# Optimization experiments

Hardware: AMD Instinct MI355X
Metric: run time of the kernel (lower is better)

## Reference

```python
import jax, jax.numpy as jnp
import numpy as np

S, B, E, H = 512, 64, 512, 512  # seq_len, batch, embed_dim, lstm_dim


def setup_inputs() -> dict:
    key = jax.random.key(0)
    ks = jax.random.split(key, 16)
    scale = 0.03

    def W(k):
        return jax.random.normal(k, (E + H, H), jnp.float32) * scale

    return {
        "embedded_tokens": jax.random.normal(ks[0], (S, B, E), jnp.float32),
        "hidden0": jnp.zeros((B, H), jnp.float32),
        "context0": jnp.zeros((B, H), jnp.float32),
        "Wf": W(ks[1]), "bf": jnp.zeros((H,), jnp.float32),
        "Wi": W(ks[2]), "bi": jnp.zeros((H,), jnp.float32),
        "Wo": W(ks[3]), "bo": jnp.zeros((H,), jnp.float32),
        "Wc": W(ks[4]), "bc": jnp.zeros((H,), jnp.float32),
        "Wmf": W(ks[5]), "bmf": jnp.zeros((H,), jnp.float32),
        "Wmi": W(ks[6]), "bmi": jnp.zeros((H,), jnp.float32),
        "seq_lengths": jax.random.randint(ks[7], (B,), 1, S + 1, jnp.int32),
    }


def reference(embedded_tokens, hidden0, context0, Wf, bf, Wi, bi, Wo, bo,
              Wc, bc, Wmf, bmf, Wmi, bmi, seq_lengths):
    # ON-LSTM recurrence, dropout p=0.0 so dropout is identity.
    def step(carry, x_t):
        h, c = carry                                   # [B,H], [B,H]
        z = jnp.concatenate([x_t, h], axis=1)          # [B, E+H]
        ft = jax.nn.sigmoid(z @ Wf + bf)
        it = jax.nn.sigmoid(z @ Wi + bi)
        ot = jax.nn.sigmoid(z @ Wo + bo)
        c_hat = jnp.tanh(z @ Wc + bc)
        mf = jnp.cumsum(jax.nn.softmax(z @ Wmf + bmf, axis=1), axis=1)  # master forget (cumax)
        mi = jnp.cumsum(jax.nn.softmax(z @ Wmi + bmi, axis=1), axis=1)  # master input (cumax)
        wt = mf * mi
        f_hat = ft * wt + (mf - wt)
        i_hat = it * wt + (mi - wt)
        c = f_hat * c + i_hat * c_hat
        h = ot * c
        return (h, c), (h, c)

    (_h, _c), (all_h, all_c) = jax.lax.scan(step, (hidden0, context0), embedded_tokens)
    # gather final valid state per example
    t_idx = seq_lengths - 1                            # [B]
    b_idx = jnp.arange(all_h.shape[1])
    state_hidden = all_h[t_idx, b_idx]                 # [B,H]
    state_context = all_c[t_idx, b_idx]                # [B,H]
    return all_h, state_hidden, state_context
```

## Files before the change

kernel.cpp:

```cpp
#include <hip/hip_runtime.h>

#define S_LEN 512
#define NWG   64
#define COLS  48
#define OUT_ALLH (512*64*512)
#define OUT_SH   (OUT_ALLH)
#define OUT_SC   (OUT_ALLH + 64*512)

#define O_WT    0ull
#define SZ_WT   (3072ull*1024*2)
#define O_BIAS  (O_WT + SZ_WT)
#define SZ_BIAS (3072ull*4)
#define O_HBF   (O_BIAS + SZ_BIAS)
#define SZ_HBF  (2ull*64*512*2)
#define O_FLAGH (O_HBF + SZ_HBF)
#define O_P     (O_FLAGH + 256)
#define SZ_P    (64ull*128*4)
#define O_XBF   (O_P + SZ_P)
#define SZ_XBF  (512ull*64*512*2)
#define WS_FULL (O_XBF + SZ_XBF)

#define L_WLDS  0
#define L_PLDS  98304
#define L_PART  132096
#define L_HBUF  134144
#define L_CBUF  136192
#define L_BLDS  138240
#define L_SLEN  138432
#define SMEM_TOTAL 138688

#define PSTR 132

typedef short bf16x8 __attribute__((ext_vector_type(8)));
typedef float f32x4  __attribute__((ext_vector_type(4)));

__device__ __forceinline__ unsigned short f2bf(float f) {
  unsigned u = __float_as_uint(f);
  u += 0x7fffu + ((u >> 16) & 1u);
  return (unsigned short)(u >> 16);
}

#define ATOM_LD(p)    __hip_atomic_load((p), __ATOMIC_RELAXED, __HIP_MEMORY_SCOPE_AGENT)
#define ATOM_ST(p, v) __hip_atomic_store((p), (v), __ATOMIC_RELAXED, __HIP_MEMORY_SCOPE_AGENT)

struct PrepArgs {
  const float* W[6]; const float* bia[6];
  const float* h0;
  unsigned short* WT; float* bias_all; unsigned short* Hbf;
  int* flagH;
};

__global__ void prep_kernel(PrepArgs a) {
  const int n = blockIdx.x, tid = threadIdx.x;
  if (n < 3072) {
    const int q = n >> 9, col = n & 511;
    const float* Wq = a.W[q];
    for (int k = tid; k < 1024; k += 256)
      a.WT[(size_t)n*1024 + k] = f2bf(Wq[k*512 + col]);
    if (tid == 0) a.bias_all[n] = a.bia[q][col];
  } else if (n < 3136) {
    const int r = n - 3072;
    for (int h = tid; h < 512; h += 256) {
      const int w = h >> 3, c = h & 7;
      a.Hbf[(size_t)(64 + w)*512 + r*8 + c] = f2bf(a.h0[r*512 + h]);
    }
  } else {
    if (tid < 64) a.flagH[tid] = 0;
  }
}

__global__ void convx_kernel(const float* __restrict__ x, unsigned short* __restrict__ xbf) {
  const size_t i = ((size_t)blockIdx.x*256 + threadIdx.x) * 4;
  float4 v = *(const float4*)(x + i);
  ushort4 r;
  r.x = f2bf(v.x); r.y = f2bf(v.y); r.z = f2bf(v.z); r.w = f2bf(v.w);
  *(ushort4*)(xbf + i) = r;
}

struct LstmArgs {
  const float* x; const unsigned short* xbf; const float* c0; const int* slen;
  const unsigned short* WT; const float* bias_all; unsigned short* Hbf;
  int* flagH; float* P; float* out;
};

__device__ __forceinline__ void gemm_one(const uint4& afr, const char* wlds,
                                         int lane, int bkc, int nt, f32x4& acc) {
  const int bcol = nt*16 + (lane & 15);
  bf16x8 b = *(const bf16x8*)(wlds + bcol*2048 + (((bkc + bcol) & 127) << 4));
  bf16x8 av = *(const bf16x8*)&afr;
  acc = __builtin_amdgcn_mfma_f32_16x16x32_bf16(av, b, acc, 0, 0, 0);
}

__device__ __forceinline__ void gemm_q3(const uint4* af, const char* wlds,
                                        int lane, int kh, f32x4* acc) {
  #pragma unroll
  for (int kt = 0; kt < 8; ++kt) {
    const int bkc = kh*32 + kt*4 + (lane >> 4);
    #pragma unroll
    for (int nt = 0; nt < 3; ++nt) gemm_one(af[kt], wlds, lane, bkc, nt, acc[nt]);
  }
}

__device__ __forceinline__ void load_xf(const LstmArgs& a, bool ux, int t, int q,
                                        int arow, int lane, uint4 xf[8]) {
  #pragma unroll
  for (int kt = 0; kt < 8; ++kt) {
    const size_t off = ((size_t)t*64 + arow)*512 + (size_t)(q*32 + kt*4 + (lane >> 4))*8;
    if (ux) {
      xf[kt] = *(const uint4*)(a.xbf + off);
    } else {
      const float* sp = a.x + off;
      float4 v0 = *(const float4*)(sp);
      float4 v1 = *(const float4*)(sp + 4);
      xf[kt].x = (unsigned)f2bf(v0.x) | ((unsigned)f2bf(v0.y) << 16);
      xf[kt].y = (unsigned)f2bf(v0.z) | ((unsigned)f2bf(v0.w) << 16);
      xf[kt].z = (unsigned)f2bf(v1.x) | ((unsigned)f2bf(v1.y) << 16);
      xf[kt].w = (unsigned)f2bf(v1.z) | ((unsigned)f2bf(v1.w) << 16);
    }
  }
}

__launch_bounds__(256, 1)
__global__ void lstm_kernel(LstmArgs a) {
  extern __shared__ char smem[];
  char*  wlds  = smem + L_WLDS;
  float* Plds  = (float*)(smem + L_PLDS);
  float* part  = (float*)(smem + L_PART);
  float* hbuf  = (float*)(smem + L_HBUF);
  float* cbuf  = (float*)(smem + L_CBUF);
  float* blds  = (float*)(smem + L_BLDS);
  int*   slenl = (int*)(smem + L_SLEN);

  const int wg = blockIdx.x, tid = threadIdx.x;
  const int lane = tid & 63, wv = tid >> 6;
  const int g = lane >> 4;
  const int c = lane & 7;
  const bool hib = (lane & 8) != 0;
  const int arow = wv*16 + (lane & 15);
  const int crow0 = wv*16 + g*4;
  const bool ux = (a.xbf != nullptr);

  for (int m = tid; m < COLS*128; m += 256) {
    const int col = m >> 7, kc = m & 127;
    const int q = col >> 3, cc = col & 7;
    uint4 v = *(const uint4*)(a.WT + ((size_t)(q*512 + wg*8 + cc))*1024 + kc*8);
    *(uint4*)(wlds + col*2048 + (((kc + col) & 127) << 4)) = v;
  }
  if (tid < COLS) { const int q = tid >> 3, cc = tid & 7; blds[tid] = a.bias_all[q*512 + wg*8 + cc]; }
  if (tid < 64) slenl[tid] = a.slen[tid];
  __syncthreads();

  const float b0 = blds[lane & 15];
  const float b1 = blds[16 + (lane & 15)];
  const float b2 = blds[32 + (lane & 15)];

  float cstv[4];
  #pragma unroll
  for (int ri = 0; ri < 4; ++ri)
    cstv[ri] = a.c0[(size_t)(crow0 + ri)*512 + wg*8 + c];

  f32x4 accC[3] = { f32x4{0,0,0,0}, f32x4{0,0,0,0}, f32x4{0,0,0,0} };
  {
    uint4 xf[8];
    load_xf(a, ux, 0, 0, arow, lane, xf);
    gemm_q3(xf, wlds, lane, 0, accC);
    load_xf(a, ux, 0, 1, arow, lane, xf);
    gemm_q3(xf, wlds, lane, 1, accC);
  }

  for (int t = 0; t < S_LEN; ++t) {
    if (tid < 64) {
      while (ATOM_LD(&a.flagH[tid]) < t)
        __builtin_amdgcn_s_sleep(1);
    }
    __syncthreads();

    const int buf = (t+1) & 1;
    uint4 hf[16];
    #pragma unroll
    for (int j = 0; j < 16; ++j) {
      const int wl = (j & 7)*4 + (lane >> 4) + ((j >> 3) << 5);
      const unsigned short* src = a.Hbf + ((size_t)(buf*64 + wl))*512 + (size_t)arow*8;
      asm volatile("global_load_dwordx4 %0, %1, off sc0 sc1" : "=v"(hf[j]) : "v"(src));
    }
    f32x4 acc2b = f32x4{0,0,0,0};
    asm volatile("s_waitcnt vmcnt(8)" ::: "memory");
    __builtin_amdgcn_sched_barrier(0);
    #pragma unroll
    for (int kt = 0; kt < 8; ++kt)
      gemm_one(hf[kt], wlds, lane, 2*32 + kt*4 + (lane >> 4), 2, accC[2]);
    asm volatile("s_waitcnt vmcnt(0)" ::: "memory");
    __builtin_amdgcn_sched_barrier(0);
    #pragma unroll
    for (int kt = 0; kt < 8; ++kt)
      gemm_one(hf[8+kt], wlds, lane, 3*32 + kt*4 + (lane >> 4), 2, acc2b);

    const unsigned ep = (unsigned)(t & 1);
    const int tn = t + 1;

    float e4[4], s4[4];
    #pragma unroll
    for (int ri = 0; ri < 4; ++ri) {
      float e = __expf(accC[2][ri] + acc2b[ri] + b2);
      e = fmaxf(e, 1e-30f);
      e4[ri] = e; s4[ri] = e;
    }
    #pragma unroll
    for (int m = 1; m < 8; m <<= 1)
      #pragma unroll
      for (int ri = 0; ri < 4; ++ri)
        s4[ri] += __shfl_xor(s4[ri], m, 64);
    if ((lane & 7) == 0) {
      const int base = wg*128 + (hib ? 64 : 0) + crow0;
      const unsigned u0 = __float_as_uint(s4[0]) | (ep << 31);
      const unsigned u1 = __float_as_uint(s4[1]) | (ep << 31);
      const unsigned u2 = __float_as_uint(s4[2]) | (ep << 31);
      const unsigned u3 = __float_as_uint(s4[3]) | (ep << 31);
      ATOM_ST((unsigned long long*)(a.P + base),     ((unsigned long long)u1 << 32) | u0);
      ATOM_ST((unsigned long long*)(a.P + base + 2), ((unsigned long long)u3 << 32) | u2);
    }

    #pragma unroll
    for (int q = 0; q < 2; ++q)
      #pragma unroll
      for (int kt = 0; kt < 8; ++kt) {
        const int bkc = (2+q)*32 + kt*4 + (lane >> 4);
        gemm_one(hf[q*8+kt], wlds, lane, bkc, 0, accC[0]);
        gemm_one(hf[q*8+kt], wlds, lane, bkc, 1, accC[1]);
      }

    f32x4 accN[3] = { f32x4{0,0,0,0}, f32x4{0,0,0,0}, f32x4{0,0,0,0} };
    uint4 xf[8];
    if (tn < S_LEN) {
      load_xf(a, ux, tn, 0, arow, lane, xf);
      gemm_q3(xf, wlds, lane, 0, accN);
    }

    float t0[4], t1[4];
    #pragma unroll
    for (int ri = 0; ri < 4; ++ri) {
      const float v0 = accC[0][ri] + b0;
      t0[ri] = __builtin_amdgcn_rcpf(1.f + __expf(-v0));
      const float v1 = accC[1][ri] + b1;
      const float e = __expf(hib ? 2.f*v1 : -v1);
      const float r = __builtin_amdgcn_rcpf(1.f + e);
      t1[ri] = hib ? (e - 1.f)*r : r;
    }

    uint4 pbuf[8];
    {
      bool ok = false;
      do {
        #pragma unroll
        for (int j = 0; j < 8; ++j) {
          const int idx = tid + j*256;
          const float* src = a.P + (size_t)idx*4;
          asm volatile("global_load_dwordx4 %0, %1, off sc0 sc1" : "=v"(pbuf[j]) : "v"(src));
        }
        asm volatile("s_waitcnt vmcnt(0)" ::: "memory");
        __builtin_amdgcn_sched_barrier(0);
        unsigned agg = ep ? 0xFFFFFFFFu : 0u;
        #pragma unroll
        for (int j = 0; j < 8; ++j) {
          if (ep) agg &= (pbuf[j].x & pbuf[j].y & pbuf[j].z & pbuf[j].w);
          else    agg |= (pbuf[j].x | pbuf[j].y | pbuf[j].z | pbuf[j].w);
        }
        ok = ((agg >> 31) == ep);
        if (!ok) __builtin_amdgcn_s_sleep(1);
      } while (!ok);
    }

    #pragma unroll
    for (int j = 0; j < 8; ++j) {
      const int idx = tid + j*256;
      const int w = idx >> 5, o = (idx & 31)*4;
      *(uint4*)((char*)Plds + ((size_t)w*PSTR + o)*4) = pbuf[j];
    }
    __syncthreads();

    {
      const int p = tid >> 1, half = tid & 1;
      float tot = 0.f, offv = 0.f;
      #pragma unroll
      for (int i = 0; i < 32; ++i) {
        const int w = half*32 + i;
        const float v = __builtin_fabsf(Plds[w*PSTR + p]);
        tot += v;
        if (w < wg) offv += v;
      }
      *(float2*)(part + tid*2) = make_float2(tot, offv);
    }
    __syncthreads();

    float m4[4];
    {
      float pr[4];
      #pragma unroll
      for (int ri = 0; ri < 4; ++ri) pr[ri] = e4[ri];
      #pragma unroll
      for (int d = 1; d < 8; d <<= 1)
        #pragma unroll
        for (int ri = 0; ri < 4; ++ri) {
          const float v = __shfl_up(pr[ri], d, 8);
          if (c >= d) pr[ri] += v;
        }
      #pragma unroll
      for (int ri = 0; ri < 4; ++ri) {
        const int p = (hib ? 64 : 0) + crow0 + ri;
        const float4 pp = *(const float4*)(part + p*4);
        const float inv = __builtin_amdgcn_rcpf(pp.x + pp.z);
        m4[ri] = ((pp.y + pp.w) + pr[ri]) * inv;
      }
    }

    float hv4[4], cn4[4];
    #pragma unroll
    for (int ri = 0; ri < 4; ++ri) {
      const float q0 = __shfl_xor(t0[ri], 8, 64);
      const float q1 = __shfl_xor(t1[ri], 8, 64);
      const float qm = __shfl_xor(m4[ri], 8, 64);
      const float f  = hib ? q0 : t0[ri];
      const float i_ = hib ? t0[ri] : q0;
      const float o  = hib ? q1 : t1[ri];
      const float ch = hib ? t1[ri] : q1;
      const float mf = hib ? qm : m4[ri];
      const float mi = hib ? m4[ri] : qm;
      const float w2 = mf * mi;
      const float cn = (f*w2 + (mf - w2))*cstv[ri] + (i_*w2 + (mi - w2))*ch;
      cstv[ri] = cn;
      cn4[ri] = cn;
      hv4[ri] = o * cn;
    }
    if (!hib) {
      #pragma unroll
      for (int ri = 0; ri < 4; ++ri) {
        hbuf[(crow0 + ri)*8 + c] = hv4[ri];
        cbuf[(crow0 + ri)*8 + c] = cn4[ri];
      }
    }
    __syncthreads();

    const int er = tid >> 2, eu = tid & 3;
    const float h0 = hbuf[er*8 + eu*2], h1 = hbuf[er*8 + eu*2 + 1];
    {
      const unsigned pk = (unsigned)f2bf(h0) | ((unsigned)f2bf(h1) << 16);
      ATOM_ST((unsigned*)(a.Hbf + ((size_t)((t & 1)*64 + wg))*512 + er*8 + eu*2), pk);
    }
    asm volatile("s_waitcnt vmcnt(0)" ::: "memory");
    __syncthreads();
    if (tid == 0) ATOM_ST(&a.flagH[wg], t+1);

    if (tn < S_LEN) {
      load_xf(a, ux, tn, 1, arow, lane, xf);
      gemm_q3(xf, wlds, lane, 1, accN);
    }

    {
      const int col = wg*8 + eu*2;
      *(float2*)(a.out + (size_t)t*32768 + er*512 + col) = make_float2(h0, h1);
      if (t == slenl[er] - 1) {
        *(float2*)(a.out + (size_t)OUT_SH + er*512 + col) = make_float2(h0, h1);
        *(float2*)(a.out + (size_t)OUT_SC + er*512 + col) =
            make_float2(cbuf[er*8 + eu*2], cbuf[er*8 + eu*2 + 1]);
      }
    }

    accC[0] = accN[0]; accC[1] = accN[1]; accC[2] = accN[2];
  }
}

extern "C" void kernel_launch(void* const* d_in, const int* in_sizes, int n_in,
                              void* d_out, int out_size, void* d_ws, size_t ws_size,
                              hipStream_t stream) {
  char* ws = (char*)d_ws;

  PrepArgs pa;
  for (int q = 0; q < 6; ++q) {
    pa.W[q]   = (const float*)d_in[3 + 2*q];
    pa.bia[q] = (const float*)d_in[4 + 2*q];
  }
  pa.h0       = (const float*)d_in[1];
  pa.WT       = (unsigned short*)(ws + O_WT);
  pa.bias_all = (float*)(ws + O_BIAS);
  pa.Hbf      = (unsigned short*)(ws + O_HBF);
  pa.flagH    = (int*)(ws + O_FLAGH);
  prep_kernel<<<3137, 256, 0, stream>>>(pa);

  const bool ux = (ws_size >= WS_FULL);
  if (ux)
    convx_kernel<<<16384, 256, 0, stream>>>((const float*)d_in[0], (unsigned short*)(ws + O_XBF));

  LstmArgs la;
  la.x        = (const float*)d_in[0];
  la.xbf      = ux ? (const unsigned short*)(ws + O_XBF) : nullptr;
  la.c0       = (const float*)d_in[2];
  la.slen     = (const int*)d_in[15];
  la.WT       = pa.WT;
  la.bias_all = pa.bias_all;
  la.Hbf      = pa.Hbf;
  la.flagH    = pa.flagH;
  la.P        = (float*)(ws + O_P);
  la.out      = (float*)d_out;

  hipFuncSetAttribute(reinterpret_cast<const void*>(lstm_kernel),
                      hipFuncAttributeMaxDynamicSharedMemorySize, SMEM_TOTAL);
  lstm_kernel<<<NWG, 256, SMEM_TOTAL, stream>>>(la);
}
```

Baseline: 4.382 ms.

## Split batch into two independent halves to overlap their recurrence phases

Splits the 64-row batch into two 32-row groups, each with its own hidden-state buffer, softmax partial-sum buffer and flag set. Two waves compute each group's recurrent GEMM while the other group's gate activations, cross-workgroup cumsum exchange and state update proceed, so one group's global synchronisation latency is meant to hide behind the other's work. Gate results move through LDS and are activated there instead of being combined via lane shuffles. In exchange there are twice as many grid-wide handshakes per step, more block barriers, and only half the waves doing MFMA work in each phase.

```diff
diff --git a/kernel.cpp b/kernel.cpp
--- a/kernel.cpp
+++ b/kernel.cpp
@@ -12,24 +12,23 @@
 #define O_BIAS  (O_WT + SZ_WT)
 #define SZ_BIAS (3072ull*4)
 #define O_HBF   (O_BIAS + SZ_BIAS)
-#define SZ_HBF  (2ull*64*512*2)
-#define O_FLAGH (O_HBF + SZ_HBF)
-#define O_P     (O_FLAGH + 256)
-#define SZ_P    (64ull*128*4)
+#define SZ_HBF  (2ull*2*64*32*8*2)
+#define O_FLAG  (O_HBF + SZ_HBF)
+#define SZ_FLAG (512ull)
+#define O_P     (O_FLAG + SZ_FLAG)
+#define SZ_P    (2ull*64*64*4)
 #define O_XBF   (O_P + SZ_P)
 #define SZ_XBF  (512ull*64*512*2)
 #define WS_FULL (O_XBF + SZ_XBF)
 
 #define L_WLDS  0
 #define L_PLDS  98304
-#define L_PART  132096
-#define L_HBUF  134144
-#define L_CBUF  136192
-#define L_BLDS  138240
-#define L_SLEN  138432
-#define SMEM_TOTAL 138688
-
-#define PSTR 132
+#define L_GATES 115712
+#define L_PART  129280
+#define L_CST   131328
+#define L_BLDS  133632
+#define L_SLEN  133824
+#define SMEM_TOTAL 134080
 
 typedef short bf16x8 __attribute__((ext_vector_type(8)));
 typedef float f32x4  __attribute__((ext_vector_type(4)));
@@ -47,7 +46,7 @@
   const float* W[6]; const float* bia[6];
   const float* h0;
   unsigned short* WT; float* bias_all; unsigned short* Hbf;
-  int* flagH;
+  int* flag;
 };
 
 __global__ void prep_kernel(PrepArgs a) {
@@ -60,12 +59,13 @@
     if (tid == 0) a.bias_all[n] = a.bia[q][col];
   } else if (n < 3136) {
     const int r = n - 3072;
+    const int g = r >> 5, rl = r & 31;
     for (int h = tid; h < 512; h += 256) {
       const int w = h >> 3, c = h & 7;
-      a.Hbf[(size_t)(64 + w)*512 + r*8 + c] = f2bf(a.h0[r*512 + h]);
+      a.Hbf[(size_t)g*32768 + 16384 + w*256 + rl*8 + c] = f2bf(a.h0[r*512 + h]);
     }
   } else {
-    if (tid < 64) a.flagH[tid] = 0;
+    if (tid < 128) a.flag[tid] = 0;
   }
 }
 
@@ -80,7 +80,7 @@
 struct LstmArgs {
   const float* x; const unsigned short* xbf; const float* c0; const int* slen;
   const unsigned short* WT; const float* bias_all; unsigned short* Hbf;
-  int* flagH; float* P; float* out;
+  int* flag; float* P; float* out;
 };
 
 __device__ __forceinline__ void gemm_one(const uint4& afr, const char* wlds,
@@ -123,21 +123,23 @@
 __launch_bounds__(256, 1)
 __global__ void lstm_kernel(LstmArgs a) {
   extern __shared__ char smem[];
-  char*  wlds  = smem + L_WLDS;
-  float* Plds  = (float*)(smem + L_PLDS);
-  float* part  = (float*)(smem + L_PART);
-  float* hbuf  = (float*)(smem + L_HBUF);
-  float* cbuf  = (float*)(smem + L_CBUF);
-  float* blds  = (float*)(smem + L_BLDS);
-  int*   slenl = (int*)(smem + L_SLEN);
+  char*  wlds   = smem + L_WLDS;
+  float* Plds   = (float*)(smem + L_PLDS);
+  float* gatesA = (float*)(smem + L_GATES);
+  float* gatesB = gatesA + 32*53;
+  float* part   = (float*)(smem + L_PART);
+  float* cstA   = (float*)(smem + L_CST);
+  float* cstB   = cstA + 32*9;
+  int*   flagA  = a.flag;
+  int*   flagB  = a.flag + 64;
+  float* blds   = (float*)(smem + L_BLDS);
+  int*   slenl  = (int*)(smem + L_SLEN);
 
   const int wg = blockIdx.x, tid = threadIdx.x;
   const int lane = tid & 63, wv = tid >> 6;
-  const int g = lane >> 4;
-  const int c = lane & 7;
-  const bool hib = (lane & 8) != 0;
-  const int arow = wv*16 + (lane & 15);
-  const int crow0 = wv*16 + g*4;
+  const int wgrp = wv >> 1;
+  const int mt = wv & 1;
+  const int arl = mt*16 + (lane & 15);
   const bool ux = (a.xbf != nullptr);
 
   for (int m = tid; m < COLS*128; m += 256) {
@@ -146,222 +148,331 @@
     uint4 v = *(const uint4*)(a.WT + ((size_t)(q*512 + wg*8 + cc))*1024 + kc*8);
     *(uint4*)(wlds + col*2048 + (((kc + col) & 127) << 4)) = v;
   }
-  if (tid < COLS) { const int q = tid >> 3, cc = tid & 7; blds[tid] = a.bias_all[q*512 + wg*8 + cc]; }
+  if (tid < COLS) blds[tid] = a.bias_all[(tid>>3)*512 + wg*8 + (tid&7)];
   if (tid < 64) slenl[tid] = a.slen[tid];
+  for (int e = tid; e < 512; e += 256) {
+    const int r = e >> 3, c = e & 7;
+    float* cs = (r < 32) ? cstA : cstB;
+    cs[(r & 31)*9 + c] = a.c0[(size_t)r*512 + wg*8 + c];
+  }
   __syncthreads();
-
-  const float b0 = blds[lane & 15];
-  const float b1 = blds[16 + (lane & 15)];
-  const float b2 = blds[32 + (lane & 15)];
-
-  float cstv[4];
-  #pragma unroll
-  for (int ri = 0; ri < 4; ++ri)
-    cstv[ri] = a.c0[(size_t)(crow0 + ri)*512 + wg*8 + c];
 
   f32x4 accC[3] = { f32x4{0,0,0,0}, f32x4{0,0,0,0}, f32x4{0,0,0,0} };
   {
     uint4 xf[8];
-    load_xf(a, ux, 0, 0, arow, lane, xf);
+    load_xf(a, ux, 0, 0, wgrp*32 + arl, lane, xf);
     gemm_q3(xf, wlds, lane, 0, accC);
-    load_xf(a, ux, 0, 1, arow, lane, xf);
+    load_xf(a, ux, 0, 1, wgrp*32 + arl, lane, xf);
     gemm_q3(xf, wlds, lane, 1, accC);
   }
 
   for (int t = 0; t < S_LEN; ++t) {
+    const unsigned ep = (unsigned)(t & 1);
+    const int buf = (t+1) & 1;
+    const int tn = t + 1;
+    uint4 hf[16];
+    uint4 xf[8];
+    f32x4 accN[3] = { f32x4{0,0,0,0}, f32x4{0,0,0,0}, f32x4{0,0,0,0} };
+    float hv0 = 0.f, hv1 = 0.f, cv0 = 0.f, cv1 = 0.f;
+
+    if (tid < 64) { while (ATOM_LD(&flagA[tid]) < t) __builtin_amdgcn_s_sleep(1); }
+    __syncthreads();
+
+    if (wgrp == 0) {
+      const unsigned short* Hb = a.Hbf + (size_t)buf*16384;
+      #pragma unroll
+      for (int j = 0; j < 16; ++j) {
+        const int kc = ((j>>3)<<5) + (j&7)*4 + (lane>>4);
+        asm volatile("global_load_dwordx4 %0, %1, off sc0 sc1"
+                     : "=v"(hf[j]) : "v"(Hb + (size_t)kc*256 + (size_t)arl*8));
+      }
+      asm volatile("s_waitcnt vmcnt(8)" ::: "memory");
+      __builtin_amdgcn_sched_barrier(0);
+      #pragma unroll
+      for (int kt = 0; kt < 8; ++kt)
+        gemm_one(hf[kt], wlds, lane, 64 + kt*4 + (lane>>4), 2, accC[2]);
+      asm volatile("s_waitcnt vmcnt(0)" ::: "memory");
+      __builtin_amdgcn_sched_barrier(0);
+      #pragma unroll
+      for (int kt = 0; kt < 8; ++kt)
+        gemm_one(hf[8+kt], wlds, lane, 96 + kt*4 + (lane>>4), 2, accC[2]);
+      #pragma unroll
+      for (int ri = 0; ri < 4; ++ri)
+        gatesA[(mt*16 + (lane>>4)*4 + ri)*53 + 32 + (lane&15)] = accC[2][ri];
+    }
+    __syncthreads();
+
     if (tid < 64) {
-      while (ATOM_LD(&a.flagH[tid]) < t)
-        __builtin_amdgcn_s_sleep(1);
-    }
-    __syncthreads();
-
-    const int buf = (t+1) & 1;
-    uint4 hf[16];
+      const int gi = tid >> 5, r = tid & 31;
+      float s = 0.f;
+      #pragma unroll
+      for (int c2 = 0; c2 < 8; ++c2) {
+        float e = __expf(gatesA[r*53 + 32 + gi*8 + c2] + blds[32 + gi*8 + c2]);
+        e = fmaxf(e, 1e-30f);
+        gatesA[r*53 + 32 + gi*8 + c2] = e;
+        s += e;
+      }
+      ATOM_ST((unsigned*)(a.P + (size_t)wg*64 + tid), __float_as_uint(s) | (ep << 31));
+    }
+
+    if (wgrp == 0) {
+      #pragma unroll
+      for (int hh = 0; hh < 2; ++hh)
+        #pragma unroll
+        for (int kt = 0; kt < 8; ++kt) {
+          const int bkc = (2+hh)*32 + kt*4 + (lane>>4);
+          gemm_one(hf[hh*8+kt], wlds, lane, bkc, 0, accC[0]);
+          gemm_one(hf[hh*8+kt], wlds, lane, bkc, 1, accC[1]);
+        }
+      #pragma unroll
+      for (int nt = 0; nt < 2; ++nt)
+        #pragma unroll
+        for (int ri = 0; ri < 4; ++ri)
+          gatesA[(mt*16 + (lane>>4)*4 + ri)*53 + nt*16 + (lane&15)] = accC[nt][ri];
+    }
+
+    if (tid < 64) { while (ATOM_LD(&flagB[tid]) < t) __builtin_amdgcn_s_sleep(1); }
+    __syncthreads();
+
+    if (wgrp == 1) {
+      const unsigned short* Hb = a.Hbf + 32768 + (size_t)buf*16384;
+      #pragma unroll
+      for (int j = 0; j < 16; ++j) {
+        const int kc = ((j>>3)<<5) + (j&7)*4 + (lane>>4);
+        asm volatile("global_load_dwordx4 %0, %1, off sc0 sc1"
+                     : "=v"(hf[j]) : "v"(Hb + (size_t)kc*256 + (size_t)arl*8));
+      }
+      asm volatile("s_waitcnt vmcnt(8)" ::: "memory");
+      __builtin_amdgcn_sched_barrier(0);
+      #pragma unroll
+      for (int kt = 0; kt < 8; ++kt)
+        gemm_one(hf[kt], wlds, lane, 64 + kt*4 + (lane>>4), 2, accC[2]);
+      asm volatile("s_waitcnt vmcnt(0)" ::: "memory");
+      __builtin_amdgcn_sched_barrier(0);
+      #pragma unroll
+      for (int kt = 0; kt < 8; ++kt)
+        gemm_one(hf[8+kt], wlds, lane, 96 + kt*4 + (lane>>4), 2, accC[2]);
+      #pragma unroll
+      for (int ri = 0; ri < 4; ++ri)
+        gatesB[(mt*16 + (lane>>4)*4 + ri)*53 + 32 + (lane&15)] = accC[2][ri];
+    }
+    __syncthreads();
+
+    if (tid < 64) {
+      const int gi = tid >> 5, r = tid & 31;
+      float s = 0.f;
+      #pragma unroll
+      for (int c2 = 0; c2 < 8; ++c2) {
+        float e = __expf(gatesB[r*53 + 32 + gi*8 + c2] + blds[32 + gi*8 + c2]);
+        e = fmaxf(e, 1e-30f);
+        gatesB[r*53 + 32 + gi*8 + c2] = e;
+        s += e;
+      }
+      ATOM_ST((unsigned*)(a.P + 4096 + (size_t)wg*64 + tid), __float_as_uint(s) | (ep << 31));
+    }
+
+    if (wgrp == 1) {
+      #pragma unroll
+      for (int hh = 0; hh < 2; ++hh)
+        #pragma unroll
+        for (int kt = 0; kt < 8; ++kt) {
+          const int bkc = (2+hh)*32 + kt*4 + (lane>>4);
+          gemm_one(hf[hh*8+kt], wlds, lane, bkc, 0, accC[0]);
+          gemm_one(hf[hh*8+kt], wlds, lane, bkc, 1, accC[1]);
+        }
+      #pragma unroll
+      for (int nt = 0; nt < 2; ++nt)
+        #pragma unroll
+        for (int ri = 0; ri < 4; ++ri)
+          gatesB[(mt*16 + (lane>>4)*4 + ri)*53 + nt*16 + (lane&15)] = accC[nt][ri];
+    }
+
     #pragma unroll
-    for (int j = 0; j < 16; ++j) {
-      const int wl = (j & 7)*4 + (lane >> 4) + ((j >> 3) << 5);
-      const unsigned short* src = a.Hbf + ((size_t)(buf*64 + wl))*512 + (size_t)arow*8;
-      asm volatile("global_load_dwordx4 %0, %1, off sc0 sc1" : "=v"(hf[j]) : "v"(src));
-    }
-    f32x4 acc2b = f32x4{0,0,0,0};
-    asm volatile("s_waitcnt vmcnt(8)" ::: "memory");
-    __builtin_amdgcn_sched_barrier(0);
-    #pragma unroll
-    for (int kt = 0; kt < 8; ++kt)
-      gemm_one(hf[kt], wlds, lane, 2*32 + kt*4 + (lane >> 4), 2, accC[2]);
-    asm volatile("s_waitcnt vmcnt(0)" ::: "memory");
-    __builtin_amdgcn_sched_barrier(0);
-    #pragma unroll
-    for (int kt = 0; kt < 8; ++kt)
-      gemm_one(hf[8+kt], wlds, lane, 3*32 + kt*4 + (lane >> 4), 2, acc2b);
-
-    const unsigned ep = (unsigned)(t & 1);
-    const int tn = t + 1;
-
-    float e4[4], s4[4];
-    #pragma unroll
-    for (int ri = 0; ri < 4; ++ri) {
-      float e = __expf(accC[2][ri] + acc2b[ri] + b2);
-      e = fmaxf(e, 1e-30f);
-      e4[ri] = e; s4[ri] = e;
-    }
-    #pragma unroll
-    for (int m = 1; m < 8; m <<= 1)
-      #pragma unroll
-      for (int ri = 0; ri < 4; ++ri)
-        s4[ri] += __shfl_xor(s4[ri], m, 64);
-    if ((lane & 7) == 0) {
-      const int base = wg*128 + (hib ? 64 : 0) + crow0;
-      const unsigned u0 = __float_as_uint(s4[0]) | (ep << 31);
-      const unsigned u1 = __float_as_uint(s4[1]) | (ep << 31);
-      const unsigned u2 = __float_as_uint(s4[2]) | (ep << 31);
-      const unsigned u3 = __float_as_uint(s4[3]) | (ep << 31);
-      ATOM_ST((unsigned long long*)(a.P + base),     ((unsigned long long)u1 << 32) | u0);
-      ATOM_ST((unsigned long long*)(a.P + base + 2), ((unsigned long long)u3 << 32) | u2);
-    }
-
-    #pragma unroll
-    for (int q = 0; q < 2; ++q)
-      #pragma unroll
-      for (int kt = 0; kt < 8; ++kt) {
-        const int bkc = (2+q)*32 + kt*4 + (lane >> 4);
-        gemm_one(hf[q*8+kt], wlds, lane, bkc, 0, accC[0]);
-        gemm_one(hf[q*8+kt], wlds, lane, bkc, 1, accC[1]);
-      }
-
-    f32x4 accN[3] = { f32x4{0,0,0,0}, f32x4{0,0,0,0}, f32x4{0,0,0,0} };
-    uint4 xf[8];
-    if (tn < S_LEN) {
-      load_xf(a, ux, tn, 0, arow, lane, xf);
-      gemm_q3(xf, wlds, lane, 0, accN);
-    }
-
-    float t0[4], t1[4];
-    #pragma unroll
-    for (int ri = 0; ri < 4; ++ri) {
-      const float v0 = accC[0][ri] + b0;
-      t0[ri] = __builtin_amdgcn_rcpf(1.f + __expf(-v0));
-      const float v1 = accC[1][ri] + b1;
-      const float e = __expf(hib ? 2.f*v1 : -v1);
-      const float r = __builtin_amdgcn_rcpf(1.f + e);
-      t1[ri] = hib ? (e - 1.f)*r : r;
-    }
-
-    uint4 pbuf[8];
+    for (int j = 0; j < 4; ++j) {
+      const int m2 = tid + j*256;
+      const int r = m2 >> 5, c2 = m2 & 31;
+      const float v = gatesA[r*53 + c2] + blds[c2];
+      const float e = __expf((c2 < 24) ? -v : 2.f*v);
+      gatesA[r*53 + c2] = (c2 < 24) ? 1.f/(1.f+e) : (e-1.f)/(e+1.f);
+    }
+
     {
+      uint4 pbuf[4];
+      const float* Pg = a.P;
       bool ok = false;
       do {
         #pragma unroll
-        for (int j = 0; j < 8; ++j) {
-          const int idx = tid + j*256;
-          const float* src = a.P + (size_t)idx*4;
-          asm volatile("global_load_dwordx4 %0, %1, off sc0 sc1" : "=v"(pbuf[j]) : "v"(src));
-        }
+        for (int j = 0; j < 4; ++j)
+          asm volatile("global_load_dwordx4 %0, %1, off sc0 sc1"
+                       : "=v"(pbuf[j]) : "v"(Pg + (size_t)tid*16 + j*4));
         asm volatile("s_waitcnt vmcnt(0)" ::: "memory");
         __builtin_amdgcn_sched_barrier(0);
         unsigned agg = ep ? 0xFFFFFFFFu : 0u;
         #pragma unroll
-        for (int j = 0; j < 8; ++j) {
+        for (int j = 0; j < 4; ++j) {
           if (ep) agg &= (pbuf[j].x & pbuf[j].y & pbuf[j].z & pbuf[j].w);
           else    agg |= (pbuf[j].x | pbuf[j].y | pbuf[j].z | pbuf[j].w);
         }
         ok = ((agg >> 31) == ep);
         if (!ok) __builtin_amdgcn_s_sleep(1);
       } while (!ok);
-    }
-
-    #pragma unroll
-    for (int j = 0; j < 8; ++j) {
-      const int idx = tid + j*256;
-      const int w = idx >> 5, o = (idx & 31)*4;
-      *(uint4*)((char*)Plds + ((size_t)w*PSTR + o)*4) = pbuf[j];
+      #pragma unroll
+      for (int j = 0; j < 4; ++j)
+        *(uint4*)(Plds + (size_t)(tid>>2)*68 + (tid&3)*16 + j*4) = pbuf[j];
     }
     __syncthreads();
 
     {
-      const int p = tid >> 1, half = tid & 1;
+      const int combo = tid >> 2, q = tid & 3;
       float tot = 0.f, offv = 0.f;
       #pragma unroll
-      for (int i = 0; i < 32; ++i) {
-        const int w = half*32 + i;
-        const float v = __builtin_fabsf(Plds[w*PSTR + p]);
+      for (int i = 0; i < 16; ++i) {
+        const int w = q*16 + i;
+        const float v = __builtin_fabsf(Plds[w*68 + combo]);
         tot += v;
         if (w < wg) offv += v;
       }
       *(float2*)(part + tid*2) = make_float2(tot, offv);
     }
     __syncthreads();
-
-    float m4[4];
+    if (tid < 64) {
+      const int gi = tid >> 5, r = tid & 31;
+      float4 p0 = *(const float4*)(part + tid*8);
+      float4 p1 = *(const float4*)(part + tid*8 + 4);
+      const float inv = 1.f / (p0.x + p0.z + p1.x + p1.z);
+      float run = p0.y + p0.w + p1.y + p1.w;
+      #pragma unroll
+      for (int c2 = 0; c2 < 8; ++c2) {
+        run += gatesA[r*53 + 32 + gi*8 + c2];
+        gatesA[r*53 + 32 + gi*8 + c2] = run * inv;
+      }
+    }
+    __syncthreads();
+
+    if (tid < 128) {
+      const int r = (tid >> 2) & 31, eu = tid & 3;
+      const float* gg = gatesA + r*53;
+      float hvv[2], cvv[2];
+      #pragma unroll
+      for (int u = 0; u < 2; ++u) {
+        const int c2 = eu*2 + u;
+        const float ft = gg[c2], it = gg[8+c2], ot = gg[16+c2], ch = gg[24+c2];
+        const float mf = gg[32+c2], mi = gg[40+c2];
+        const float w2 = mf * mi;
+        const float cn = (ft*w2 + (mf - w2))*cstA[r*9+c2] + (it*w2 + (mi - w2))*ch;
+        cstA[r*9+c2] = cn; cvv[u] = cn; hvv[u] = ot*cn;
+      }
+      hv0 = hvv[0]; hv1 = hvv[1]; cv0 = cvv[0]; cv1 = cvv[1];
+      const unsigned pk = (unsigned)f2bf(hvv[0]) | ((unsigned)f2bf(hvv[1]) << 16);
+      ATOM_ST((unsigned*)(a.Hbf + (size_t)(t&1)*16384 + wg*256 + r*8 + eu*2), pk);
+    }
+    asm volatile("s_waitcnt vmcnt(0)" ::: "memory");
+    __syncthreads();
+    if (tid == 0) ATOM_ST(&flagA[wg], t+1);
+
+    #pragma unroll
+    for (int j = 0; j < 4; ++j) {
+      const int m2 = tid + j*256;
+      const int r = m2 >> 5, c2 = m2 & 31;
+      const float v = gatesB[r*53 + c2] + blds[c2];
+      const float e = __expf((c2 < 24) ? -v : 2.f*v);
+      gatesB[r*53 + c2] = (c2 < 24) ? 1.f/(1.f+e) : (e-1.f)/(e+1.f);
+    }
+    if (wgrp == 0 && tn < S_LEN) {
+      load_xf(a, ux, tn, 0, arl, lane, xf);
+      gemm_q3(xf, wlds, lane, 0, accN);
+      load_xf(a, ux, tn, 1, arl, lane, xf);
+      gemm_q3(xf, wlds, lane, 1, accN);
+    }
+
     {
-      float pr[4];
-      #pragma unroll
-      for (int ri = 0; ri < 4; ++ri) pr[ri] = e4[ri];
-      #pragma unroll
-      for (int d = 1; d < 8; d <<= 1)
-        #pragma unroll
-        for (int ri = 0; ri < 4; ++ri) {
-          const float v = __shfl_up(pr[ri], d, 8);
-          if (c >= d) pr[ri] += v;
+      uint4 pbuf[4];
+      const float* Pg = a.P + 4096;
+      bool ok = false;
+      do {
+        #pragma unroll
+        for (int j = 0; j < 4; ++j)
+          asm volatile("global_load_dwordx4 %0, %1, off sc0 sc1"
+                       : "=v"(pbuf[j]) : "v"(Pg + (size_t)tid*16 + j*4));
+        asm volatile("s_waitcnt vmcnt(0)" ::: "memory");
+        __builtin_amdgcn_sched_barrier(0);
+        unsigned agg = ep ? 0xFFFFFFFFu : 0u;
+        #pragma unroll
+        for (int j = 0; j < 4; ++j) {
+          if (ep) agg &= (pbuf[j].x & pbuf[j].y & pbuf[j].z & pbuf[j].w);
+          else    agg |= (pbuf[j].x | pbuf[j].y | pbuf[j].z | pbuf[j].w);
         }
-      #pragma unroll
-      for (int ri = 0; ri < 4; ++ri) {
-        const int p = (hib ? 64 : 0) + crow0 + ri;
-        const float4 pp = *(const float4*)(part + p*4);
-        const float inv = __builtin_amdgcn_rcpf(pp.x + pp.z);
-        m4[ri] = ((pp.y + pp.w) + pr[ri]) * inv;
-      }
-    }
-
-    float hv4[4], cn4[4];
-    #pragma unroll
-    for (int ri = 0; ri < 4; ++ri) {
-      const float q0 = __shfl_xor(t0[ri], 8, 64);
-      const float q1 = __shfl_xor(t1[ri], 8, 64);
-      const float qm = __shfl_xor(m4[ri], 8, 64);
-      const float f  = hib ? q0 : t0[ri];
-      const float i_ = hib ? t0[ri] : q0;
-      const float o  = hib ? q1 : t1[ri];
-      const float ch = hib ? t1[ri] : q1;
-      const float mf = hib ? qm : m4[ri];
-      const float mi = hib ? m4[ri] : qm;
-      const float w2 = mf * mi;
-      const float cn = (f*w2 + (mf - w2))*cstv[ri] + (i_*w2 + (mi - w2))*ch;
-      cstv[ri] = cn;
-      cn4[ri] = cn;
-      hv4[ri] = o * cn;
-    }
-    if (!hib) {
-      #pragma unroll
-      for (int ri = 0; ri < 4; ++ri) {
-        hbuf[(crow0 + ri)*8 + c] = hv4[ri];
-        cbuf[(crow0 + ri)*8 + c] = cn4[ri];
-      }
-    }
-    __syncthreads();
-
-    const int er = tid >> 2, eu = tid & 3;
-    const float h0 = hbuf[er*8 + eu*2], h1 = hbuf[er*8 + eu*2 + 1];
+        ok = ((agg >> 31) == ep);
+        if (!ok) __builtin_amdgcn_s_sleep(1);
+      } while (!ok);
+      #pragma unroll
+      for (int j = 0; j < 4; ++j)
+        *(uint4*)(Plds + (size_t)(tid>>2)*68 + (tid&3)*16 + j*4) = pbuf[j];
+    }
+    __syncthreads();
+
     {
-      const unsigned pk = (unsigned)f2bf(h0) | ((unsigned)f2bf(h1) << 16);
-      ATOM_ST((unsigned*)(a.Hbf + ((size_t)((t & 1)*64 + wg))*512 + er*8 + eu*2), pk);
+      const int combo = tid >> 2, q = tid & 3;
+      float tot = 0.f, offv = 0.f;
+      #pragma unroll
+      for (int i = 0; i < 16; ++i) {
+        const int w = q*16 + i;
+        const float v = __builtin_fabsf(Plds[w*68 + combo]);
+        tot += v;
+        if (w < wg) offv += v;
+      }
+      *(float2*)(part + tid*2) = make_float2(tot, offv);
+    }
+    __syncthreads();
+    if (tid < 64) {
+      const int gi = tid >> 5, r = tid & 31;
+      float4 p0 = *(const float4*)(part + tid*8);
+      float4 p1 = *(const float4*)(part + tid*8 + 4);
+      const float inv = 1.f / (p0.x + p0.z + p1.x + p1.z);
+      float run = p0.y + p0.w + p1.y + p1.w;
+      #pragma unroll
+      for (int c2 = 0; c2 < 8; ++c2) {
+        run += gatesB[r*53 + 32 + gi*8 + c2];
+        gatesB[r*53 + 32 + gi*8 + c2] = run * inv;
+      }
+    }
+    __syncthreads();
+
+    if (tid >= 128) {
+      const int r = (tid >> 2) & 31, eu = tid & 3;
+      const float* gg = gatesB + r*53;
+      float hvv[2], cvv[2];
+      #pragma unroll
+      for (int u = 0; u < 2; ++u) {
+        const int c2 = eu*2 + u;
+        const float ft = gg[c2], it = gg[8+c2], ot = gg[16+c2], ch = gg[24+c2];
+        const float mf = gg[32+c2], mi = gg[40+c2];
+        const float w2 = mf * mi;
+        const float cn = (ft*w2 + (mf - w2))*cstB[r*9+c2] + (it*w2 + (mi - w2))*ch;
+        cstB[r*9+c2] = cn; cvv[u] = cn; hvv[u] = ot*cn;
+      }
+      hv0 = hvv[0]; hv1 = hvv[1]; cv0 = cvv[0]; cv1 = cvv[1];
+      const unsigned pk = (unsigned)f2bf(hvv[0]) | ((unsigned)f2bf(hvv[1]) << 16);
+      ATOM_ST((unsigned*)(a.Hbf + 32768 + (size_t)(t&1)*16384 + wg*256 + r*8 + eu*2), pk);
     }
     asm volatile("s_waitcnt vmcnt(0)" ::: "memory");
     __syncthreads();
-    if (tid == 0) ATOM_ST(&a.flagH[wg], t+1);
-
-    if (tn < S_LEN) {
-      load_xf(a, ux, tn, 1, arow, lane, xf);
+    if (tid == 0) ATOM_ST(&flagB[wg], t+1);
+
+    if (wgrp == 1 && tn < S_LEN) {
+      load_xf(a, ux, tn, 0, 32 + arl, lane, xf);
+      gemm_q3(xf, wlds, lane, 0, accN);
+      load_xf(a, ux, tn, 1, 32 + arl, lane, xf);
       gemm_q3(xf, wlds, lane, 1, accN);
     }
-
     {
+      const int g = tid >> 7, r = (tid >> 2) & 31, eu = tid & 3;
+      const int abr = g*32 + r;
       const int col = wg*8 + eu*2;
-      *(float2*)(a.out + (size_t)t*32768 + er*512 + col) = make_float2(h0, h1);
-      if (t == slenl[er] - 1) {
-        *(float2*)(a.out + (size_t)OUT_SH + er*512 + col) = make_float2(h0, h1);
-        *(float2*)(a.out + (size_t)OUT_SC + er*512 + col) =
-            make_float2(cbuf[er*8 + eu*2], cbuf[er*8 + eu*2 + 1]);
+      *(float2*)(a.out + (size_t)t*32768 + abr*512 + col) = make_float2(hv0, hv1);
+      if (t == slenl[abr] - 1) {
+        *(float2*)(a.out + (size_t)OUT_SH + abr*512 + col) = make_float2(hv0, hv1);
+        *(float2*)(a.out + (size_t)OUT_SC + abr*512 + col) = make_float2(cv0, cv1);
       }
     }
 
@@ -383,7 +494,7 @@
   pa.WT       = (unsigned short*)(ws + O_WT);
   pa.bias_all = (float*)(ws + O_BIAS);
   pa.Hbf      = (unsigned short*)(ws + O_HBF);
-  pa.flagH    = (int*)(ws + O_FLAGH);
+  pa.flag     = (int*)(ws + O_FLAG);
   prep_kernel<<<3137, 256, 0, stream>>>(pa);
 
   const bool ux = (ws_size >= WS_FULL);
@@ -398,7 +509,7 @@
   la.WT       = pa.WT;
   la.bias_all = pa.bias_all;
   la.Hbf      = pa.Hbf;
-  la.flagH    = pa.flagH;
+  la.flag     = pa.flag;
   la.P        = (float*)(ws + O_P);
   la.out      = (float*)d_out;
 
```

Result: slower. 7.109 ms (+62.2%).
